# Kernel optimization log

Measured on AMD Instinct MI355X. Metric: run time of the kernel, lower is better.

## Reference

```python
import jax, jax.numpy as jnp
import numpy as np

B, T, C = 4, 2048, 768
N_HEAD = 12
HS = C // N_HEAD

def setup_inputs() -> dict:
    key = jax.random.key(0)
    ks = jax.random.split(key, 5)
    s = 0.02
    return {
        "x": jax.random.normal(ks[0], (B, T, C), dtype=jnp.float32),
        "w_attn": jax.random.normal(ks[1], (C, 3 * C), dtype=jnp.float32) * s,
        "b_attn": jnp.zeros((3 * C,), dtype=jnp.float32),
        "w_proj": jax.random.normal(ks[2], (C, C), dtype=jnp.float32) * s,
        "b_proj": jnp.zeros((C,), dtype=jnp.float32),
    }

def reference(x, w_attn, b_attn, w_proj, b_proj):
    Bx, Tx, Cx = x.shape
    qkv = x @ w_attn + b_attn                      # [B,T,3C]
    q, k, v = jnp.split(qkv, 3, axis=-1)
    # [B,H,T,hs]
    q = q.reshape(Bx, Tx, N_HEAD, HS).transpose(0, 2, 1, 3)
    k = k.reshape(Bx, Tx, N_HEAD, HS).transpose(0, 2, 1, 3)
    v = v.reshape(Bx, Tx, N_HEAD, HS).transpose(0, 2, 1, 3)
    att = jnp.einsum('bhqd,bhkd->bhqk', q, k) * (1.0 / jnp.sqrt(jnp.float32(HS)))
    mask = jnp.tril(jnp.ones((Tx, Tx), dtype=bool))  # causal
    att = jnp.where(mask, att, jnp.float32(-jnp.inf))
    att = jax.nn.softmax(att, axis=-1)
    y = jnp.einsum('bhqk,bhkd->bhqd', att, v)
    y = y.transpose(0, 2, 1, 3).reshape(Bx, Tx, Cx)
    return y @ w_proj + b_proj
```

## Files before the change

### kernel.cpp

```cpp
#include <hip/hip_runtime.h>

#define BB 4
#define TT 2048
#define CC 768
#define QKVW 2304
#define NHH 12
#define HSS 64
#define NQT64 (TT / 64)

typedef __attribute__((ext_vector_type(4))) float floatx4;
typedef __attribute__((ext_vector_type(8))) short shortx8;
typedef __attribute__((ext_vector_type(4))) short shortx4;

__device__ __forceinline__ unsigned short f2bf(float f) {
  union { float f; unsigned int u; } cv; cv.f = f;
  unsigned int u = cv.u;
  u += 0x7FFFu + ((u >> 16) & 1u);
  return (unsigned short)(u >> 16);
}
__device__ __forceinline__ unsigned short bfp(float f) {
  union { float f; unsigned int u; } cv; cv.f = f;
  return (unsigned short)((cv.u + 0x8000u) >> 16);
}
__device__ __forceinline__ unsigned short bft(float f) {
  union { float f; unsigned int u; } cv; cv.f = f;
  return (unsigned short)(cv.u >> 16);
}

__device__ __forceinline__ void async_copy16(const void* g, void* l) {
  __builtin_amdgcn_global_load_lds(
      (const __attribute__((address_space(1))) unsigned int*)g,
      (__attribute__((address_space(3))) unsigned int*)l, 16, 0, 0);
}

__global__ __launch_bounds__(256)
void prep_fused(const float* __restrict__ x, unsigned short* __restrict__ xb, int n4,
                const float* __restrict__ wa, unsigned short* __restrict__ wta,
                const float* __restrict__ wp, unsigned short* __restrict__ wtp) {
  __shared__ short tile[64 * 68];
  const int bid = blockIdx.x;
  const int tid = threadIdx.x;
  if (bid < 1024) {
    int i = bid * 256 + tid;
    const int stride = 1024 * 256;
    for (; i < n4; i += stride) {
      float4 v = ((const float4*)x)[i];
      shortx4 s;
      s.x = (short)f2bf(v.x); s.y = (short)f2bf(v.y);
      s.z = (short)f2bf(v.z); s.w = (short)f2bf(v.w);
      ((shortx4*)xb)[i] = s;
    }
    return;
  }
  const float* w; unsigned short* wt; int N, n0, k0;
  if (bid < 1456) {
    const int t = bid - 1024;
    w = wa; wt = wta; N = QKVW; n0 = (t % 36) * 64; k0 = (t / 36) * 64;
  } else {
    const int t = bid - 1456;
    w = wp; wt = wtp; N = CC;   n0 = (t % 12) * 64; k0 = (t / 12) * 64;
  }
  const int K = CC;
  {
    const int tr = tid >> 4, tc = (tid & 15) * 4;
#pragma unroll
    for (int i = 0; i < 4; ++i) {
      float4 v = *(const float4*)(w + (size_t)(k0 + tr + 16 * i) * N + n0 + tc);
      short* d = &tile[(tr + 16 * i) * 68 + tc];
      d[0] = (short)f2bf(v.x); d[1] = (short)f2bf(v.y);
      d[2] = (short)f2bf(v.z); d[3] = (short)f2bf(v.w);
    }
  }
  __syncthreads();
  {
    const int wr = tid >> 3, wc = (tid & 7) * 8;
#pragma unroll
    for (int j = 0; j < 2; ++j) {
      const int n = wr + 32 * j;
      shortx8 s;
#pragma unroll
      for (int e = 0; e < 8; ++e) s[e] = tile[(wc + e) * 68 + n];
      *(shortx8*)(wt + (size_t)(n0 + n) * K + k0 + wc) = s;
    }
  }
}

__global__ __launch_bounds__(256)
void transpose_v(const unsigned short* __restrict__ qkv, unsigned short* __restrict__ Vt) {
  __shared__ short tile[64 * 72];
  const int t0 = blockIdx.x * 64;
  const int bh = blockIdx.y;
  const int b = bh / NHH, h = bh % NHH;
  const int tid = threadIdx.x;
  {
    const int tr = tid >> 3, tc = (tid & 7) * 8;
#pragma unroll
    for (int i = 0; i < 2; ++i) {
      shortx8 v = *(const shortx8*)(qkv + ((size_t)(b * TT + t0 + tr + 32 * i)) * QKVW + 2 * CC + h * HSS + tc);
      *(shortx8*)&tile[(tr + 32 * i) * 72 + tc] = v;
    }
  }
  __syncthreads();
  {
    const int dr = tid >> 3, tc = (tid & 7) * 8;
    const int base = (tc & 32) + ((tc >> 3) & 3) * 4;
#pragma unroll
    for (int j = 0; j < 2; ++j) {
      const int d = dr + 32 * j;
      shortx8 s;
#pragma unroll
      for (int e = 0; e < 8; ++e)
        s[e] = tile[(base + (e >> 2) * 16 + (e & 3)) * 72 + d];
      *(shortx8*)(Vt + ((size_t)bh * HSS + d) * TT + t0 + tc) = s;
    }
  }
}

template<bool OUT_BF16, bool QSCALE>
__global__ __launch_bounds__(256)
void gemm_tn(const unsigned short* __restrict__ A, const unsigned short* __restrict__ Bt,
             const float* __restrict__ bias, void* __restrict__ Cp, int M, int N, int K) {
  __shared__ short As[3][128 * 32];
  __shared__ short Bs[3][128 * 32];
  const int tid = threadIdx.x, lane = tid & 63, wave = tid >> 6;
  const int row = lane & 15, quad = lane >> 4;
  const int wm = (wave >> 1) * 64, wn = (wave & 1) * 64;
  const int m0 = blockIdx.x * 128, n0 = blockIdx.y * 128;

  floatx4 acc[4][4] = {};

  const int lr = lane >> 2;
  const int csrc = (lane & 3) ^ ((lr >> 1) & 3);
  const int sr = wave * 32 + lr;
  const unsigned short* aP = A + (size_t)(m0 + sr) * K + csrc * 8;
  const unsigned short* bP = Bt + (size_t)(n0 + sr) * K + csrc * 8;
  const int sOff = (wave * 32) * 32;

  const int qsw = (quad ^ ((row >> 1) & 3)) * 8;

  const int nk = K >> 5;

  auto stage = [&](int t, int bi) {
#pragma unroll
    for (int i = 0; i < 2; ++i) {
      async_copy16(aP + (size_t)(16 * i) * K + t * 32, &As[bi][sOff + i * 512]);
      async_copy16(bP + (size_t)(16 * i) * K + t * 32, &Bs[bi][sOff + i * 512]);
    }
  };

  stage(0, 0);
  if (nk > 1) stage(1, 1);
  int cb = 0;
  for (int t = 0; t < nk; ++t) {
    __builtin_amdgcn_sched_barrier(0);
    __builtin_amdgcn_s_barrier();
    __builtin_amdgcn_sched_barrier(0);
    int pb = cb + 2; if (pb >= 3) pb -= 3;
    if (t + 2 < nk) {
      stage(t + 2, pb);
      asm volatile("s_waitcnt vmcnt(8)" ::: "memory");
    } else if (t + 1 < nk) {
      asm volatile("s_waitcnt vmcnt(4)" ::: "memory");
    } else {
      asm volatile("s_waitcnt vmcnt(0)" ::: "memory");
    }
    __builtin_amdgcn_sched_barrier(0);
    {
      shortx8 af[4], bf[4];
#pragma unroll
      for (int g = 0; g < 4; ++g) {
        af[g] = *(const shortx8*)&As[cb][(wm + g * 16 + row) * 32 + qsw];
        bf[g] = *(const shortx8*)&Bs[cb][(wn + g * 16 + row) * 32 + qsw];
      }
#pragma unroll
      for (int mg = 0; mg < 4; ++mg)
#pragma unroll
        for (int ng = 0; ng < 4; ++ng)
          acc[mg][ng] = __builtin_amdgcn_mfma_f32_16x16x32_bf16(af[mg], bf[ng], acc[mg][ng], 0, 0, 0);
    }
    cb = (cb + 1 == 3) ? 0 : cb + 1;
  }

#pragma unroll
  for (int mg = 0; mg < 4; ++mg) {
    const int m = m0 + wm + mg * 16 + quad * 4;
#pragma unroll
    for (int ng = 0; ng < 4; ++ng) {
      const int n = n0 + wn + ng * 16 + row;
      const float bv = bias[n];
      const float scl = (QSCALE && n < CC) ? 0.180336881f : 1.0f;
#pragma unroll
      for (int r = 0; r < 4; ++r) {
        const float val = (acc[mg][ng][r] + bv) * scl;
        if (OUT_BF16) ((unsigned short*)Cp)[(size_t)(m + r) * N + n] = f2bf(val);
        else          ((float*)Cp)[(size_t)(m + r) * N + n] = val;
      }
    }
  }
}

__global__ __launch_bounds__(256)
void attn_kernel(const unsigned short* __restrict__ qkv, const unsigned short* __restrict__ Vt,
                 unsigned short* __restrict__ y) {
  __shared__ short Ksh[3][64 * 64];
  __shared__ short Vsh[3][64 * 64];

  const int id = blockIdx.x;
  const int xcd = id & 7;
  const int slot = id >> 3;
  const int qt = NQT64 - 1 - slot / 6;
  const int gl = slot % 6;
  const int g = xcd * 6 + gl;
  const int h = g % NHH, b = g / NHH;
  const int bh = b * NHH + h;
  const int tid = threadIdx.x, lane = tid & 63, wave = tid >> 6;
  const int row = lane & 15, quad = lane >> 4;
  const int qhalf = wave & 1;
  const int khalf = wave >> 1;

  const unsigned short* kSrc = qkv + ((size_t)(b * TT)) * QKVW + CC + h * HSS;
  const unsigned short* vSrc = Vt + ((size_t)bh * HSS) * TT;

  const shortx8 ones8 = {(short)0x3F80, (short)0x3F80, (short)0x3F80, (short)0x3F80,
                         (short)0x3F80, (short)0x3F80, (short)0x3F80, (short)0x3F80};

  const int qb0 = qt * 64 + qhalf * 32;
  const int nk = qt + 1;

  const int lr8 = lane >> 3;
  const int csw = ((lane & 7) ^ lr8) * 8;
  size_t kOff[2], vOff[2];
#pragma unroll
  for (int i = 0; i < 2; ++i) {
    const int r = wave * 16 + i * 8 + lr8;
    kOff[i] = (size_t)r * QKVW + csw;
    vOff[i] = (size_t)r * TT + csw;
  }
  const int sBase = (wave * 16) * 64;

  const int r7 = row & 7;
  int kR[2][2], vR[4];
#pragma unroll
  for (int mg = 0; mg < 2; ++mg) {
    const int krow = khalf * 32 + mg * 16 + row;
    kR[mg][0] = krow * 64 + ((quad ^ r7) * 8);
    kR[mg][1] = krow * 64 + (((quad + 4) ^ r7) * 8);
  }
#pragma unroll
  for (int dg = 0; dg < 4; ++dg)
    vR[dg] = (dg * 16 + row) * 64 + (((khalf * 4 + quad) ^ r7) * 8);

  shortx8 qf[2][2];
#pragma unroll
  for (int qg = 0; qg < 2; ++qg) {
    const unsigned short* qp = qkv + ((size_t)(b * TT) + qb0 + qg * 16 + row) * QKVW + h * HSS;
    qf[qg][0] = *(const shortx8*)(qp + quad * 8);
    qf[qg][1] = *(const shortx8*)(qp + 32 + quad * 8);
  }
  asm volatile("s_waitcnt vmcnt(0)" ::: "memory");

  floatx4 lf[2] = {(floatx4)(0.0f), (floatx4)(0.0f)};
  floatx4 o[2][4];
#pragma unroll
  for (int qg = 0; qg < 2; ++qg)
#pragma unroll
    for (int dg = 0; dg < 4; ++dg) o[qg][dg] = (floatx4)(0.0f);

  auto stage = [&](int t, int bi) {
#pragma unroll
    for (int i = 0; i < 2; ++i) {
      async_copy16(kSrc + (size_t)(t * 64) * QKVW + kOff[i], &Ksh[bi][sBase + i * 512]);
      async_copy16(vSrc + (size_t)(t * 64) + vOff[i],        &Vsh[bi][sBase + i * 512]);
    }
  };

  stage(0, 0);
  if (nk > 1) stage(1, 1);
  int cb = 0;
  for (int kt = 0; kt < nk; ++kt) {
    __builtin_amdgcn_sched_barrier(0);
    __builtin_amdgcn_s_barrier();
    __builtin_amdgcn_sched_barrier(0);
    int pb = cb + 2; if (pb >= 3) pb -= 3;
    if (kt + 2 < nk) {
      stage(kt + 2, pb);
      asm volatile("s_waitcnt vmcnt(8)" ::: "memory");
    } else if (kt + 1 < nk) {
      asm volatile("s_waitcnt vmcnt(4)" ::: "memory");
    } else {
      asm volatile("s_waitcnt vmcnt(0)" ::: "memory");
    }
    __builtin_amdgcn_sched_barrier(0);
    {
      const short* Kc = &Ksh[cb][0];
      const short* Vc = &Vsh[cb][0];
      __builtin_amdgcn_s_setprio(1);
      shortx4 pfr[2][2];
#pragma unroll
      for (int mg = 0; mg < 2; ++mg) {
        const shortx8 kf0 = *(const shortx8*)&Kc[kR[mg][0]];
        const shortx8 kf1 = *(const shortx8*)&Kc[kR[mg][1]];
#pragma unroll
        for (int qg = 0; qg < 2; ++qg) {
          floatx4 t = __builtin_amdgcn_mfma_f32_16x16x32_bf16(kf0, qf[qg][0], (floatx4)(0.0f), 0, 0, 0);
          t = __builtin_amdgcn_mfma_f32_16x16x32_bf16(kf1, qf[qg][1], t, 0, 0, 0);
          if (kt == qt) {
            const int kg = kt * 64 + khalf * 32 + mg * 16 + quad * 4;
            const int qv = qb0 + qg * 16 + row;
#pragma unroll
            for (int r = 0; r < 4; ++r)
              if (kg + r > qv) t[r] = -1e30f;
          }
          shortx4 pk;
#pragma unroll
          for (int r = 0; r < 4; ++r) pk[r] = (short)bft(__builtin_amdgcn_exp2f(t[r]));
          pfr[qg][mg] = pk;
        }
      }
      shortx8 pk8[2];
#pragma unroll
      for (int qg = 0; qg < 2; ++qg) {
        pk8[qg] = __builtin_shufflevector(pfr[qg][0], pfr[qg][1], 0, 1, 2, 3, 4, 5, 6, 7);
        lf[qg] = __builtin_amdgcn_mfma_f32_16x16x32_bf16(pk8[qg], ones8, lf[qg], 0, 0, 0);
      }
#pragma unroll
      for (int dg = 0; dg < 4; ++dg) {
        const shortx8 vf = *(const shortx8*)&Vc[vR[dg]];
#pragma unroll
        for (int qg = 0; qg < 2; ++qg)
          o[qg][dg] = __builtin_amdgcn_mfma_f32_16x16x32_bf16(pk8[qg], vf, o[qg][dg], 0, 0, 0);
      }
      __builtin_amdgcn_s_setprio(0);
    }
    cb = (cb + 1 == 3) ? 0 : cb + 1;
  }
  __syncthreads();

  floatx4* red4 = (floatx4*)(&Ksh[0][0]);
  const int rbase = (qhalf * 64 + lane) * 11;
  if (khalf) {
#pragma unroll
    for (int qg = 0; qg < 2; ++qg) {
#pragma unroll
      for (int dg = 0; dg < 4; ++dg) red4[rbase + qg * 4 + dg] = o[qg][dg];
      red4[rbase + 8 + qg] = lf[qg];
    }
  }
  __syncthreads();
  if (!khalf) {
#pragma unroll
    for (int qg = 0; qg < 2; ++qg) {
#pragma unroll
      for (int dg = 0; dg < 4; ++dg) o[qg][dg] += red4[rbase + qg * 4 + dg];
      lf[qg] += red4[rbase + 8 + qg];
    }
#pragma unroll
    for (int qg = 0; qg < 2; ++qg) {
#pragma unroll
      for (int r = 0; r < 4; ++r) {
        const float lo = 1.0f / lf[qg][r];
        unsigned short* yp = y + ((size_t)(b * TT) + qb0 + qg * 16 + quad * 4 + r) * CC + h * HSS;
#pragma unroll
        for (int dg = 0; dg < 4; ++dg)
          yp[dg * 16 + row] = bfp(o[qg][dg][r] * lo);
      }
    }
  }
}

extern "C" void kernel_launch(void* const* d_in, const int* in_sizes, int n_in,
                              void* d_out, int out_size, void* d_ws, size_t ws_size,
                              hipStream_t stream) {
  const float* x      = (const float*)d_in[0];
  const float* w_attn = (const float*)d_in[1];
  const float* b_attn = (const float*)d_in[2];
  const float* w_proj = (const float*)d_in[3];
  const float* b_proj = (const float*)d_in[4];
  float* out = (float*)d_out;

  char* ws = (char*)d_ws;
  unsigned short* xb  = (unsigned short*)ws;
  unsigned short* y   = (unsigned short*)ws;
  unsigned short* qkv = (unsigned short*)(ws + 12582912);
  unsigned short* wta = (unsigned short*)(ws + 50331648);
  unsigned short* Vt  = (unsigned short*)(ws + 50331648);
  unsigned short* wtp = (unsigned short*)(ws + 62914560);

  const int M = BB * TT;

  prep_fused<<<1600, 256, 0, stream>>>(x, xb, (M * CC) / 4, w_attn, wta, w_proj, wtp);

  gemm_tn<true, true><<<dim3(M / 128, QKVW / 128), 256, 0, stream>>>(
      xb, wta, b_attn, (void*)qkv, M, QKVW, CC);

  transpose_v<<<dim3(TT / 64, BB * NHH), 256, 0, stream>>>(qkv, Vt);

  attn_kernel<<<dim3(NQT64 * NHH * BB), 256, 0, stream>>>(qkv, Vt, y);

  gemm_tn<false, false><<<dim3(M / 128, CC / 128), 256, 0, stream>>>(
      y, wtp, b_proj, (void*)out, M, CC, CC);
}
```

Measured before the change: 195.5 us.

## Load GEMM B operand directly from global into registers, bypassing LDS

The B tile is no longer staged through shared memory. Each wave loads its B fragments straight from global memory into registers one k-step ahead, double-buffered in two register arrays in a loop unrolled by two, while A keeps the triple-buffered async LDS pipeline. This removes the LDS footprint and LDS reads for B, but each pair of waves sharing a wn column now fetches the same B data redundantly from global/L2, and the wait counts are retuned to match.

```diff
diff --git a/kernel.cpp b/kernel.cpp
--- a/kernel.cpp
+++ b/kernel.cpp
@@ -121,7 +121,6 @@
 void gemm_tn(const unsigned short* __restrict__ A, const unsigned short* __restrict__ Bt,
              const float* __restrict__ bias, void* __restrict__ Cp, int M, int N, int K) {
   __shared__ short As[3][128 * 32];
-  __shared__ short Bs[3][128 * 32];
   const int tid = threadIdx.x, lane = tid & 63, wave = tid >> 6;
   const int row = lane & 15, quad = lane >> 4;
   const int wm = (wave >> 1) * 64, wn = (wave & 1) * 64;
@@ -133,53 +132,70 @@
   const int csrc = (lane & 3) ^ ((lr >> 1) & 3);
   const int sr = wave * 32 + lr;
   const unsigned short* aP = A + (size_t)(m0 + sr) * K + csrc * 8;
-  const unsigned short* bP = Bt + (size_t)(n0 + sr) * K + csrc * 8;
   const int sOff = (wave * 32) * 32;
 
+  const unsigned short* bP = Bt + (size_t)(n0 + wn + row) * K + quad * 8;
+
   const int qsw = (quad ^ ((row >> 1) & 3)) * 8;
 
   const int nk = K >> 5;
 
-  auto stage = [&](int t, int bi) {
-#pragma unroll
-    for (int i = 0; i < 2; ++i) {
+  auto stageA = [&](int t, int bi) {
+#pragma unroll
+    for (int i = 0; i < 2; ++i)
       async_copy16(aP + (size_t)(16 * i) * K + t * 32, &As[bi][sOff + i * 512]);
-      async_copy16(bP + (size_t)(16 * i) * K + t * 32, &Bs[bi][sOff + i * 512]);
-    }
   };
 
-  stage(0, 0);
-  if (nk > 1) stage(1, 1);
+  shortx8 bA[4], bB[4];
+
+  stageA(0, 0);
+  stageA(1, 1);
+#pragma unroll
+  for (int g = 0; g < 4; ++g)
+    bA[g] = *(const shortx8*)(bP + (size_t)(g * 16) * K);
+
+#define GSTEP(T, BCUR, BNXT, CBV)                                              \
+  do {                                                                         \
+    __builtin_amdgcn_sched_barrier(0);                                         \
+    __builtin_amdgcn_s_barrier();        \
+    __builtin_amdgcn_sched_barrier(0);                                         \
+    int pb_ = (CBV) + 2; if (pb_ >= 3) pb_ -= 3;                               \
+    if ((T) + 2 < nk) stageA((T) + 2, pb_);                                    \
+    __builtin_amdgcn_sched_barrier(0);                                         \
+    if ((T) + 1 < nk) {                                                        \
+      _Pragma("unroll")                                                        \
+      for (int g = 0; g < 4; ++g)                                              \
+        BNXT[g] = *(const shortx8*)(bP + (size_t)(g * 16) * K + ((T) + 1) * 32);\
+    }                                                                          \
+    __builtin_amdgcn_sched_barrier(0);                                         \
+    if ((T) + 2 < nk)      asm volatile("s_waitcnt vmcnt(6)" ::: "memory");    \
+    else if ((T) + 1 < nk) asm volatile("s_waitcnt vmcnt(4)" ::: "memory");    \
+    else                   asm volatile("s_waitcnt vmcnt(0)" ::: "memory");    \
+    __builtin_amdgcn_sched_barrier(0);                                         \
+    {                                                                          \
+      shortx8 af_[4];                                                          \
+      _Pragma("unroll")                                                        \
+      for (int g = 0; g < 4; ++g)                                              \
+        af_[g] = *(const shortx8*)&As[CBV][(wm + g * 16 + row) * 32 + qsw];    \
+      _Pragma("unroll")                                                        \
+      for (int mg = 0; mg < 4; ++mg)                                           \
+        _Pragma("unroll")                                                      \
+        for (int ng = 0; ng < 4; ++ng)                                         \
+          acc[mg][ng] = __builtin_amdgcn_mfma_f32_16x16x32_bf16(               \
+              af_[mg], BCUR[ng], acc[mg][ng], 0, 0, 0);                        \
+    }                                                                          \
+  } while (0)
+
   int cb = 0;
-  for (int t = 0; t < nk; ++t) {
-    __builtin_amdgcn_sched_barrier(0);
-    __builtin_amdgcn_s_barrier();
-    __builtin_amdgcn_sched_barrier(0);
-    int pb = cb + 2; if (pb >= 3) pb -= 3;
-    if (t + 2 < nk) {
-      stage(t + 2, pb);
-      asm volatile("s_waitcnt vmcnt(8)" ::: "memory");
-    } else if (t + 1 < nk) {
-      asm volatile("s_waitcnt vmcnt(4)" ::: "memory");
-    } else {
-      asm volatile("s_waitcnt vmcnt(0)" ::: "memory");
-    }
-    __builtin_amdgcn_sched_barrier(0);
-    {
-      shortx8 af[4], bf[4];
-#pragma unroll
-      for (int g = 0; g < 4; ++g) {
-        af[g] = *(const shortx8*)&As[cb][(wm + g * 16 + row) * 32 + qsw];
-        bf[g] = *(const shortx8*)&Bs[cb][(wn + g * 16 + row) * 32 + qsw];
-      }
-#pragma unroll
-      for (int mg = 0; mg < 4; ++mg)
-#pragma unroll
-        for (int ng = 0; ng < 4; ++ng)
-          acc[mg][ng] = __builtin_amdgcn_mfma_f32_16x16x32_bf16(af[mg], bf[ng], acc[mg][ng], 0, 0, 0);
-    }
+  for (int tt = 0; tt < nk; tt += 2) {
+    GSTEP(tt, bA, bB, cb);
     cb = (cb + 1 == 3) ? 0 : cb + 1;
-  }
+    if (tt + 1 < nk) {
+      GSTEP(tt + 1, bB, bA, cb);
+      cb = (cb + 1 == 3) ? 0 : cb + 1;
+    }
+  }
+#undef GSTEP
 
 #pragma unroll
   for (int mg = 0; mg < 4; ++mg) {
```

Result: slower. 239.3 us (+22.4%).

## Widen GEMM tile to 128x192 and switch to double-buffered pipeline

Applied to the files above, without the earlier changes.

Widens the GEMM block tile from 128x128 to 128x192, so each wave computes a 64x96 sub-tile with 4x6 MFMA accumulators. The shared-memory pipeline drops from triple to double buffering, with a barrier before and after each compute step. The larger tile raises MFMA work per LDS load and cuts the block count for both GEMMs. In exchange it uses more registers, may lower occupancy, and with only one stage of prefetch it hides less load latency.

```diff
diff --git a/kernel.cpp b/kernel.cpp
--- a/kernel.cpp
+++ b/kernel.cpp
@@ -120,21 +120,21 @@
 __global__ __launch_bounds__(256)
 void gemm_tn(const unsigned short* __restrict__ A, const unsigned short* __restrict__ Bt,
              const float* __restrict__ bias, void* __restrict__ Cp, int M, int N, int K) {
-  __shared__ short As[3][128 * 32];
-  __shared__ short Bs[3][128 * 32];
+  __shared__ short As[2][128 * 32];
+  __shared__ short Bs[2][192 * 32];
   const int tid = threadIdx.x, lane = tid & 63, wave = tid >> 6;
   const int row = lane & 15, quad = lane >> 4;
-  const int wm = (wave >> 1) * 64, wn = (wave & 1) * 64;
-  const int m0 = blockIdx.x * 128, n0 = blockIdx.y * 128;
-
-  floatx4 acc[4][4] = {};
+  const int wm = (wave >> 1) * 64, wn = (wave & 1) * 96;
+  const int m0 = blockIdx.x * 128, n0 = blockIdx.y * 192;
+
+  floatx4 acc[4][6] = {};
 
   const int lr = lane >> 2;
   const int csrc = (lane & 3) ^ ((lr >> 1) & 3);
-  const int sr = wave * 32 + lr;
-  const unsigned short* aP = A + (size_t)(m0 + sr) * K + csrc * 8;
-  const unsigned short* bP = Bt + (size_t)(n0 + sr) * K + csrc * 8;
-  const int sOff = (wave * 32) * 32;
+  const unsigned short* aP = A + (size_t)(m0 + wave * 32 + lr) * K + csrc * 8;
+  const unsigned short* bP = Bt + (size_t)(n0 + wave * 48 + lr) * K + csrc * 8;
+  const int aOff = (wave * 32) * 32;
+  const int bOff = (wave * 48) * 32;
 
   const int qsw = (quad ^ ((row >> 1) & 3)) * 8;
 
@@ -142,50 +142,50 @@
 
   auto stage = [&](int t, int bi) {
 #pragma unroll
-    for (int i = 0; i < 2; ++i) {
-      async_copy16(aP + (size_t)(16 * i) * K + t * 32, &As[bi][sOff + i * 512]);
-      async_copy16(bP + (size_t)(16 * i) * K + t * 32, &Bs[bi][sOff + i * 512]);
-    }
+    for (int i = 0; i < 2; ++i)
+      async_copy16(aP + (size_t)(16 * i) * K + t * 32, &As[bi][aOff + i * 512]);
+#pragma unroll
+    for (int i = 0; i < 3; ++i)
+      async_copy16(bP + (size_t)(16 * i) * K + t * 32, &Bs[bi][bOff + i * 512]);
   };
 
   stage(0, 0);
-  if (nk > 1) stage(1, 1);
   int cb = 0;
   for (int t = 0; t < nk; ++t) {
-    __builtin_amdgcn_sched_barrier(0);
-    __builtin_amdgcn_s_barrier();
-    __builtin_amdgcn_sched_barrier(0);
-    int pb = cb + 2; if (pb >= 3) pb -= 3;
-    if (t + 2 < nk) {
-      stage(t + 2, pb);
-      asm volatile("s_waitcnt vmcnt(8)" ::: "memory");
-    } else if (t + 1 < nk) {
-      asm volatile("s_waitcnt vmcnt(4)" ::: "memory");
+    if (t + 1 < nk) {
+      stage(t + 1, cb ^ 1);
+      asm volatile("s_waitcnt vmcnt(5)" ::: "memory");
     } else {
       asm volatile("s_waitcnt vmcnt(0)" ::: "memory");
     }
     __builtin_amdgcn_sched_barrier(0);
+    __builtin_amdgcn_s_barrier();
+    __builtin_amdgcn_sched_barrier(0);
     {
-      shortx8 af[4], bf[4];
-#pragma unroll
-      for (int g = 0; g < 4; ++g) {
+      shortx8 af[4], bf[6];
+#pragma unroll
+      for (int g = 0; g < 4; ++g)
         af[g] = *(const shortx8*)&As[cb][(wm + g * 16 + row) * 32 + qsw];
+#pragma unroll
+      for (int g = 0; g < 6; ++g)
         bf[g] = *(const shortx8*)&Bs[cb][(wn + g * 16 + row) * 32 + qsw];
-      }
 #pragma unroll
       for (int mg = 0; mg < 4; ++mg)
 #pragma unroll
-        for (int ng = 0; ng < 4; ++ng)
+        for (int ng = 0; ng < 6; ++ng)
           acc[mg][ng] = __builtin_amdgcn_mfma_f32_16x16x32_bf16(af[mg], bf[ng], acc[mg][ng], 0, 0, 0);
     }
-    cb = (cb + 1 == 3) ? 0 : cb + 1;
+    __builtin_amdgcn_sched_barrier(0);
+    __builtin_amdgcn_s_barrier();
+    __builtin_amdgcn_sched_barrier(0);
+    cb ^= 1;
   }
 
 #pragma unroll
   for (int mg = 0; mg < 4; ++mg) {
     const int m = m0 + wm + mg * 16 + quad * 4;
 #pragma unroll
-    for (int ng = 0; ng < 4; ++ng) {
+    for (int ng = 0; ng < 6; ++ng) {
       const int n = n0 + wn + ng * 16 + row;
       const float bv = bias[n];
       const float scl = (QSCALE && n < CC) ? 0.180336881f : 1.0f;
@@ -390,13 +390,13 @@
 
   prep_fused<<<1600, 256, 0, stream>>>(x, xb, (M * CC) / 4, w_attn, wta, w_proj, wtp);
 
-  gemm_tn<true, true><<<dim3(M / 128, QKVW / 128), 256, 0, stream>>>(
+  gemm_tn<true, true><<<dim3(M / 128, QKVW / 192), 256, 0, stream>>>(
       xb, wta, b_attn, (void*)qkv, M, QKVW, CC);
 
   transpose_v<<<dim3(TT / 64, BB * NHH), 256, 0, stream>>>(qkv, Vt);
 
   attn_kernel<<<dim3(NQT64 * NHH * BB), 256, 0, stream>>>(qkv, Vt, y);
 
-  gemm_tn<false, false><<<dim3(M / 128, CC / 128), 256, 0, stream>>>(
+  gemm_tn<false, false><<<dim3(M / 128, CC / 192), 256, 0, stream>>>(
       y, wtp, b_proj, (void*)out, M, CC, CC);
 }
```

Result: slower. 203.2 us (+3.9%).
